# Optimization experiments

Measured on AMD Instinct MI355X. Metric: run time of the kernel, lower is better.

The kernel has to match this reference:

```python
import jax, jax.numpy as jnp
import numpy as np

N, E, D, H = 50000, 800000, 128, 64


def _norm_adj(edge_index, num_nodes):
    # add self loops, then w_ij = d_i^{-1/2} d_j^{-1/2} with deg = in-degree of col
    loops = jnp.arange(num_nodes)
    row = jnp.concatenate([edge_index[0], loops])
    col = jnp.concatenate([edge_index[1], loops])
    deg = jax.ops.segment_sum(jnp.ones_like(col, dtype=jnp.float32), col, num_segments=num_nodes)
    dinv = jnp.where(deg > 0, jax.lax.rsqrt(deg), 0.0)
    w = dinv[row] * dinv[col]
    return row, col, w


def _spmm(row, col, w, x, num_nodes):
    # y[row] += w * x[col]  (torch.sparse.mm(adj, x))
    return jax.ops.segment_sum(w[:, None] * x[col], row, num_segments=num_nodes)


def setup_inputs() -> dict:
    key = jax.random.key(0)
    ks = jax.random.split(key, 8)
    inp = {
        "x": jax.random.normal(ks[0], (N, D), dtype=jnp.float32),
        "edge_index": jax.random.randint(ks[1], (2, E), 0, N),
        "num_nodes": N,
    }
    # per-branch, per-layer Linear weights stored as [in, hid] (x @ W)
    wk = jax.random.split(ks[2], 6)
    s = 0.05
    inp["homo_W0"] = jax.random.normal(wk[0], (D, H), dtype=jnp.float32) * s
    inp["homo_W1"] = jax.random.normal(wk[1], (H, H), dtype=jnp.float32) * s
    inp["full_W0"] = jax.random.normal(wk[2], (D, H), dtype=jnp.float32) * s
    inp["full_W1"] = jax.random.normal(wk[3], (H, H), dtype=jnp.float32) * s
    inp["het_W0"] = jax.random.normal(wk[4], (D, H), dtype=jnp.float32) * s
    inp["het_W1"] = jax.random.normal(wk[5], (H, H), dtype=jnp.float32) * s
    for name in ("homo_a0", "homo_a1", "full_a0", "full_a1", "het_a0", "het_a1",
                 "w_homo", "w_full", "w_hetero"):
        inp[name] = jnp.float32(1.0)
    return inp


def reference(x, edge_index, num_nodes,
              homo_W0, homo_W1, full_W0, full_W1, het_W0, het_W1,
              homo_a0, homo_a1, full_a0, full_a1, het_a0, het_a1,
              w_homo, w_full, w_hetero):
    row, col, w = _norm_adj(edge_index, num_nodes)

    def homo_layer(h, W, a):
        return jax.nn.relu(a * (_spmm(row, col, w, h, num_nodes) @ W))

    def full_layer(h, W, a):
        return jax.nn.relu(a * (h @ W))

    def het_layer(h, W, a):
        # L = I - A  =>  L @ h = h - A @ h
        return jax.nn.relu(a * ((h - _spmm(row, col, w, h, num_nodes)) @ W))

    h_homo = homo_layer(homo_layer(x, homo_W0, homo_a0), homo_W1, homo_a1)
    h_full = full_layer(full_layer(x, full_W0, full_a0), full_W1, full_a1)
    h_het = het_layer(het_layer(x, het_W0, het_a0), het_W1, het_a1)
    combined = w_homo * h_homo + w_full * h_full + w_hetero * h_het
    return (combined, h_homo, h_full, h_het)
```

## Files before the change

kernel.cpp:

```cpp
#include <hip/hip_runtime.h>


typedef __attribute__((ext_vector_type(8))) short short8;
typedef __attribute__((ext_vector_type(4))) float f32x4;

static __device__ __forceinline__ unsigned short f2bf(float f) {
    unsigned int u = __float_as_uint(f);
    u += 0x7FFFu + ((u >> 16) & 1u);
    return (unsigned short)(u >> 16);
}
static __device__ __forceinline__ float bflo(unsigned int pv) {
    return __uint_as_float(pv << 16);
}
static __device__ __forceinline__ float bfhi(unsigned int pv) {
    return __uint_as_float(pv & 0xFFFF0000u);
}

#define PSHIFT 7
#define PSIZE  128
#define NPART_MAX 400
#define PCAP   3072
#define ACHUNK 6272

__global__ __launch_bounds__(256) void wpackT_kernel(
    const float* __restrict__ w0, const float* __restrict__ w1,
    const float* __restrict__ w2, unsigned short* __restrict__ out)
{
    const int i = blockIdx.x * 256 + threadIdx.x;
    if (i >= 3 * 64 * 128) return;
    const int b   = i >> 13;
    const int col = (i >> 7) & 63;
    const int k   = i & 127;
    const float* __restrict__ w = (b == 0) ? w0 : ((b == 1) ? w1 : w2);
    out[i] = f2bf(w[k * 64 + col]);
}

__global__ __launch_bounds__(256) void radix_kernel(
    const int* __restrict__ ei, int E, int npart,
    int* __restrict__ gcnt_r, int* __restrict__ gcnt_c,
    unsigned int* __restrict__ rbuf, unsigned short* __restrict__ cbuf)
{
    __shared__ int hist_r[NPART_MAX], lofs_r[NPART_MAX], resv_r[NPART_MAX];
    __shared__ int hist_c[NPART_MAX], lofs_c[NPART_MAX], resv_c[NPART_MAX];
    __shared__ int seg_r[16], seg_c[16];
    __shared__ unsigned int   sr[ACHUNK];
    __shared__ unsigned short sc[ACHUNK];
    const int tid = threadIdx.x;
    const int e0 = blockIdx.x * ACHUNK;
    const int e1 = (e0 + ACHUNK < E) ? e0 + ACHUNK : E;
    const int cnt = e1 - e0;
    if (cnt <= 0) return;

    for (int i = tid; i < npart; i += 256) { hist_r[i] = 0; hist_c[i] = 0; }
    __syncthreads();

    for (int e = e0 + tid; e < e1; e += 256) {
        const int r = ei[e], c = ei[E + e];
        atomicAdd(&hist_r[r >> PSHIFT], 1);
        atomicAdd(&hist_c[c >> PSHIFT], 1);
    }
    __syncthreads();

    const int SEG = (npart + 7) / 8;
    if (tid < 8) {
        int s = 0;
        const int a = tid * SEG, b = (a + SEG < npart) ? a + SEG : npart;
        for (int i = a; i < b; ++i) { lofs_r[i] = s; s += hist_r[i]; }
        seg_r[tid] = s;
    } else if (tid >= 64 && tid < 72) {
        const int t = tid - 64;
        int s = 0;
        const int a = t * SEG, b = (a + SEG < npart) ? a + SEG : npart;
        for (int i = a; i < b; ++i) { lofs_c[i] = s; s += hist_c[i]; }
        seg_c[t] = s;
    }
    __syncthreads();
    if (tid == 0) {
        int s = 0;
        for (int k = 0; k < 8; ++k) { const int t = seg_r[k]; seg_r[k] = s; s += t; }
    } else if (tid == 64) {
        int s = 0;
        for (int k = 0; k < 8; ++k) { const int t = seg_c[k]; seg_c[k] = s; s += t; }
    }
    __syncthreads();
    for (int i = tid; i < npart; i += 256) {
        lofs_r[i] += seg_r[i / SEG];
        lofs_c[i] += seg_c[i / SEG];
    }
    __syncthreads();

    for (int i = tid; i < npart; i += 256) {
        resv_r[i] = atomicAdd(&gcnt_r[i], hist_r[i]);
        resv_c[i] = atomicAdd(&gcnt_c[i], hist_c[i]);
        hist_r[i] = 0; hist_c[i] = 0;
    }
    __syncthreads();

    for (int e = e0 + tid; e < e1; e += 256) {
        const int r = ei[e], c = ei[E + e];
        const int pr = r >> PSHIFT, pc = c >> PSHIFT;
        const int jr = lofs_r[pr] + atomicAdd(&hist_r[pr], 1);
        const int jc = lofs_c[pc] + atomicAdd(&hist_c[pc], 1);
        sr[jr] = ((unsigned int)r << 16) | (unsigned int)c;
        sc[jc] = (unsigned short)c;
    }
    __syncthreads();

    for (int j = tid; j < cnt; j += 256) {
        const unsigned int rc = sr[j];
        const int p = (int)(rc >> 16) >> PSHIFT;
        const int idx = resv_r[p] + (j - lofs_r[p]);
        if (idx < PCAP) rbuf[(size_t)p * PCAP + idx] = rc;
    }
    for (int j = tid; j < cnt; j += 256) {
        const unsigned short cv = sc[j];
        const int p = (int)cv >> PSHIFT;
        const int idx = resv_c[p] + (j - lofs_c[p]);
        if (idx < PCAP) cbuf[(size_t)p * PCAP + idx] = cv;
    }
}

__global__ __launch_bounds__(256) void bucket_kernel(
    const unsigned int* __restrict__ rbuf, const unsigned short* __restrict__ cbuf,
    const int* __restrict__ gcnt_r, const int* __restrict__ gcnt_c, int N,
    unsigned short* __restrict__ bucket, int* __restrict__ cur,
    float* __restrict__ dinv)
{
    __shared__ unsigned short sbucket[PSIZE * 64];
    __shared__ int scur[PSIZE], sdeg[PSIZE];
    const int tid = threadIdx.x;
    const int p = blockIdx.x;
    const int lo = p << PSHIFT;
    const int sl = (lo + PSIZE < N) ? PSIZE : N - lo;
    if (sl <= 0) return;

    for (int i = tid; i < sl; i += 256) { scur[i] = 0; sdeg[i] = 0; }
    __syncthreads();

    int cnt_r = gcnt_r[p]; if (cnt_r > PCAP) cnt_r = PCAP;
    int cnt_c = gcnt_c[p]; if (cnt_c > PCAP) cnt_c = PCAP;

    for (int e = tid; e < cnt_r; e += 256) {
        const unsigned int rc = rbuf[(size_t)p * PCAP + e];
        const int local = (int)(rc >> 16) - lo;
        const int pos = atomicAdd(&scur[local], 1);
        if (pos < 64) sbucket[local * 64 + pos] = (unsigned short)(rc & 0xFFFFu);
    }
    for (int e = tid; e < cnt_c; e += 256) {
        atomicAdd(&sdeg[(int)cbuf[(size_t)p * PCAP + e] - lo], 1);
    }
    __syncthreads();

    for (int i = tid; i < sl; i += 256) {
        cur[lo + i]  = scur[i];
        dinv[lo + i] = 1.0f / sqrtf((float)sdeg[i] + 1.0f);
    }
    unsigned int* gb = (unsigned int*)(bucket + (size_t)lo * 64);
    const unsigned int* sb = (const unsigned int*)sbucket;
    for (int i = tid; i < sl * 32; i += 256) gb[i] = sb[i];
}

__global__ __launch_bounds__(256) void gemm_l1_kernel(
    const float* __restrict__ x, const unsigned short* __restrict__ Wt,
    unsigned short* __restrict__ Pb, float* __restrict__ full1,
    const float* __restrict__ alphaF, int N)
{
    __shared__ __align__(16) unsigned short sx[64 * 136];
    const int tid = threadIdx.x;
    const int row0 = blockIdx.x * 64;

    #pragma unroll
    for (int j = 0; j < 8; ++j) {
        const int idx = j * 256 + tid;
        const int row = idx >> 5;
        const int c4  = idx & 31;
        float4 v = make_float4(0.f, 0.f, 0.f, 0.f);
        if (row0 + row < N) v = ((const float4*)x)[(size_t)(row0 + row) * 32 + c4];
        const unsigned int lo = (unsigned int)f2bf(v.x) | ((unsigned int)f2bf(v.y) << 16);
        const unsigned int hi = (unsigned int)f2bf(v.z) | ((unsigned int)f2bf(v.w) << 16);
        *(uint2*)&sx[row * 136 + c4 * 4] = make_uint2(lo, hi);
    }
    __syncthreads();

    const int lane = tid & 63;
    const int w = tid >> 6;
    const int g = lane >> 4;
    const int m = lane & 15;
    const float alpha = alphaF[0];

    short8 afr[4];
    #pragma unroll
    for (int kk = 0; kk < 4; ++kk)
        afr[kk] = *(const short8*)&sx[(16 * w + m) * 136 + kk * 32 + g * 8];

    const int rbase = row0 + 16 * w + g * 4;

    #pragma unroll 1
    for (int b = 0; b < 3; ++b) {
        const unsigned short* __restrict__ Wb = Wt + b * 8192;
        f32x4 acc0 = {0.f, 0.f, 0.f, 0.f};
        f32x4 acc1 = {0.f, 0.f, 0.f, 0.f};
        f32x4 acc2 = {0.f, 0.f, 0.f, 0.f};
        f32x4 acc3 = {0.f, 0.f, 0.f, 0.f};
        #pragma unroll
        for (int kk = 0; kk < 4; ++kk) {
            const unsigned short* wk = Wb + m * 128 + kk * 32 + g * 8;
            const short8 b0 = *(const short8*)(wk);
            const short8 b1 = *(const short8*)(wk + 16 * 128);
            const short8 b2 = *(const short8*)(wk + 32 * 128);
            const short8 b3 = *(const short8*)(wk + 48 * 128);
            acc0 = __builtin_amdgcn_mfma_f32_16x16x32_bf16(afr[kk], b0, acc0, 0, 0, 0);
            acc1 = __builtin_amdgcn_mfma_f32_16x16x32_bf16(afr[kk], b1, acc1, 0, 0, 0);
            acc2 = __builtin_amdgcn_mfma_f32_16x16x32_bf16(afr[kk], b2, acc2, 0, 0, 0);
            acc3 = __builtin_amdgcn_mfma_f32_16x16x32_bf16(afr[kk], b3, acc3, 0, 0, 0);
        }
        #pragma unroll
        for (int j = 0; j < 4; ++j) {
            const int row = rbase + j;
            if (row < N) {
                if (b < 2) {
                    unsigned short* p = Pb + (size_t)row * 128 + b * 64 + m;
                    p[0]  = f2bf(acc0[j]);
                    p[16] = f2bf(acc1[j]);
                    p[32] = f2bf(acc2[j]);
                    p[48] = f2bf(acc3[j]);
                } else {
                    float* p = full1 + (size_t)row * 64 + m;
                    p[0]  = fmaxf(alpha * acc0[j], 0.f);
                    p[16] = fmaxf(alpha * acc1[j], 0.f);
                    p[32] = fmaxf(alpha * acc2[j], 0.f);
                    p[48] = fmaxf(alpha * acc3[j], 0.f);
                }
            }
        }
    }
}

__global__ __launch_bounds__(256) void gemm_l2_kernel(
    const float* __restrict__ in0, const float* __restrict__ in1,
    const float* __restrict__ in2,
    const float* __restrict__ w0, const float* __restrict__ w1,
    const float* __restrict__ w2,
    unsigned short* __restrict__ Qb, float* __restrict__ outF,
    const float* __restrict__ alphaF, int N)
{
    __shared__ float sxT[64][129];
    __shared__ float sW[64 * 64];
    const int b = blockIdx.y;
    const float* __restrict__ in = (b == 0) ? in0 : ((b == 1) ? in1 : in2);
    const float* __restrict__ W  = (b == 0) ? w0  : ((b == 1) ? w1  : w2);
    const int tid = threadIdx.x;
    const int row0 = blockIdx.x * 128;

    {
        const float4* __restrict__ w4 = (const float4*)W;
        float4* sw4 = (float4*)sW;
        #pragma unroll
        for (int j = 0; j < 4; ++j) sw4[j * 256 + tid] = w4[j * 256 + tid];
    }
    if (row0 + 128 <= N) {
        const float4* __restrict__ in4 = (const float4*)(in + (size_t)row0 * 64);
        #pragma unroll
        for (int j = 0; j < 8; ++j) {
            const int idx = j * 256 + tid;
            const int row = idx >> 4;
            const int kc4 = idx & 15;
            const float4 v = in4[idx];
            sxT[4 * kc4 + 0][row] = v.x;
            sxT[4 * kc4 + 1][row] = v.y;
            sxT[4 * kc4 + 2][row] = v.z;
            sxT[4 * kc4 + 3][row] = v.w;
        }
    } else {
        for (int j = 0; j < 8; ++j) {
            const int idx = j * 256 + tid;
            const int row = idx >> 4;
            const int kc4 = idx & 15;
            float4 v = make_float4(0.f, 0.f, 0.f, 0.f);
            if (row0 + row < N) v = ((const float4*)in)[(size_t)(row0 + row) * 16 + kc4];
            sxT[4 * kc4 + 0][row] = v.x;
            sxT[4 * kc4 + 1][row] = v.y;
            sxT[4 * kc4 + 2][row] = v.z;
            sxT[4 * kc4 + 3][row] = v.w;
        }
    }
    __syncthreads();

    const int tx = tid & 15;
    const int ty = tid >> 4;
    float acc[8][4];
    #pragma unroll
    for (int r = 0; r < 8; ++r)
        #pragma unroll
        for (int c = 0; c < 4; ++c) acc[r][c] = 0.f;

    #pragma unroll 2
    for (int k = 0; k < 64; ++k) {
        const float4 wv = *(const float4*)&sW[k * 64 + 4 * tx];
        const float4 xa = *(const float4*)&sxT[k][8 * ty];
        const float4 xb = *(const float4*)&sxT[k][8 * ty + 4];
        const float xr[8] = { xa.x, xa.y, xa.z, xa.w, xb.x, xb.y, xb.z, xb.w };
        #pragma unroll
        for (int r = 0; r < 8; ++r) {
            acc[r][0] = fmaf(xr[r], wv.x, acc[r][0]);
            acc[r][1] = fmaf(xr[r], wv.y, acc[r][1]);
            acc[r][2] = fmaf(xr[r], wv.z, acc[r][2]);
            acc[r][3] = fmaf(xr[r], wv.w, acc[r][3]);
        }
    }

    const float alpha = alphaF[0];
    #pragma unroll
    for (int r = 0; r < 8; ++r) {
        const int row = row0 + 8 * ty + r;
        if (row < N) {
            if (b < 2) {
                uint2 o;
                o.x = (unsigned int)f2bf(acc[r][0]) | ((unsigned int)f2bf(acc[r][1]) << 16);
                o.y = (unsigned int)f2bf(acc[r][2]) | ((unsigned int)f2bf(acc[r][3]) << 16);
                ((uint2*)Qb)[(size_t)row * 32 + b * 16 + tx] = o;
            } else {
                float4 o = make_float4(fmaxf(alpha * acc[r][0], 0.f),
                                       fmaxf(alpha * acc[r][1], 0.f),
                                       fmaxf(alpha * acc[r][2], 0.f),
                                       fmaxf(alpha * acc[r][3], 0.f));
                ((float4*)outF)[(size_t)row * 16 + tx] = o;
            }
        }
    }
}

__global__ __launch_bounds__(256) void spmm1_kernel(
    const unsigned short* __restrict__ Pb, const unsigned short* __restrict__ bucket,
    const int* __restrict__ cnt, const float* __restrict__ dinv,
    float* __restrict__ homo1, float* __restrict__ het1,
    const float* __restrict__ aH, const float* __restrict__ aT, int N)
{
    const int i = blockIdx.x * 4 + (threadIdx.x >> 6);
    if (i >= N) return;
    const int lane = threadIdx.x & 63;
    const int g  = lane >> 4;
    const int fl = lane & 15;
    const uint4* __restrict__ P16 = (const uint4*)Pb;
    const float di = dinv[i];
    const uint4 us = P16[(size_t)i * 16 + fl];
    float ps[8];
    ps[0] = bflo(us.x); ps[1] = bfhi(us.x); ps[2] = bflo(us.y); ps[3] = bfhi(us.y);
    ps[4] = bflo(us.z); ps[5] = bfhi(us.z); ps[6] = bflo(us.w); ps[7] = bfhi(us.w);
    int n = cnt[i]; if (n > 64) n = 64;
    const unsigned int* __restrict__ bp = (const unsigned int*)(bucket + (size_t)i * 64);
    float acc[8];
    #pragma unroll
    for (int j = 0; j < 8; ++j) acc[j] = 0.f;
    for (int k0 = 0; k0 < n; k0 += 4) {
        const int k = k0 + g;
        const unsigned int pw = bp[(k0 >> 1) + (g >> 1)];
        const bool act = (k < n);
        const int craw = (int)((g & 1) ? (pw >> 16) : (pw & 0xFFFFu));
        const int c = act ? craw : i;
        const float dc = act ? dinv[c] : 0.f;
        const uint4 u = P16[(size_t)c * 16 + fl];
        acc[0] = fmaf(dc, bflo(u.x), acc[0]); acc[1] = fmaf(dc, bfhi(u.x), acc[1]);
        acc[2] = fmaf(dc, bflo(u.y), acc[2]); acc[3] = fmaf(dc, bfhi(u.y), acc[3]);
        acc[4] = fmaf(dc, bflo(u.z), acc[4]); acc[5] = fmaf(dc, bfhi(u.z), acc[5]);
        acc[6] = fmaf(dc, bflo(u.w), acc[6]); acc[7] = fmaf(dc, bfhi(u.w), acc[7]);
    }
    float y[8];
    #pragma unroll
    for (int j = 0; j < 8; ++j) {
        acc[j] += __shfl_xor(acc[j], 16);
        acc[j] += __shfl_xor(acc[j], 32);
        y[j] = di * (acc[j] + di * ps[j]);
    }
    if (lane < 8) {
        const float a = aH[0];
        float4* dst = (float4*)(homo1 + (size_t)i * 64 + 8 * lane);
        dst[0] = make_float4(fmaxf(a * y[0], 0.f), fmaxf(a * y[1], 0.f),
                             fmaxf(a * y[2], 0.f), fmaxf(a * y[3], 0.f));
        dst[1] = make_float4(fmaxf(a * y[4], 0.f), fmaxf(a * y[5], 0.f),
                             fmaxf(a * y[6], 0.f), fmaxf(a * y[7], 0.f));
    } else if (lane < 16) {
        const float a = aT[0];
        float4* dst = (float4*)(het1 + (size_t)i * 64 + 8 * (lane - 8));
        dst[0] = make_float4(fmaxf(a * (ps[0] - y[0]), 0.f), fmaxf(a * (ps[1] - y[1]), 0.f),
                             fmaxf(a * (ps[2] - y[2]), 0.f), fmaxf(a * (ps[3] - y[3]), 0.f));
        dst[1] = make_float4(fmaxf(a * (ps[4] - y[4]), 0.f), fmaxf(a * (ps[5] - y[5]), 0.f),
                             fmaxf(a * (ps[6] - y[6]), 0.f), fmaxf(a * (ps[7] - y[7]), 0.f));
    }
}

__global__ __launch_bounds__(256) void spmm2_kernel(
    const unsigned short* __restrict__ Qb, const unsigned short* __restrict__ bucket,
    const int* __restrict__ cnt, const float* __restrict__ dinv,
    const float* __restrict__ full2,
    float* __restrict__ outComb, float* __restrict__ outHomo, float* __restrict__ outHet,
    const float* __restrict__ aH, const float* __restrict__ aT,
    const float* __restrict__ wH, const float* __restrict__ wF, const float* __restrict__ wT,
    int N)
{
    const int i = blockIdx.x * 4 + (threadIdx.x >> 6);
    if (i >= N) return;
    const int lane = threadIdx.x & 63;
    const int g  = lane >> 4;
    const int fl = lane & 15;
    const uint4* __restrict__ Q16 = (const uint4*)Qb;
    const float di = dinv[i];
    const uint4 us = Q16[(size_t)i * 16 + fl];
    float ps[8];
    ps[0] = bflo(us.x); ps[1] = bfhi(us.x); ps[2] = bflo(us.y); ps[3] = bfhi(us.y);
    ps[4] = bflo(us.z); ps[5] = bfhi(us.z); ps[6] = bflo(us.w); ps[7] = bfhi(us.w);
    int n = cnt[i]; if (n > 64) n = 64;
    const unsigned int* __restrict__ bp = (const unsigned int*)(bucket + (size_t)i * 64);
    float acc[8];
    #pragma unroll
    for (int j = 0; j < 8; ++j) acc[j] = 0.f;
    for (int k0 = 0; k0 < n; k0 += 4) {
        const int k = k0 + g;
        const unsigned int pw = bp[(k0 >> 1) + (g >> 1)];
        const bool act = (k < n);
        const int craw = (int)((g & 1) ? (pw >> 16) : (pw & 0xFFFFu));
        const int c = act ? craw : i;
        const float dc = act ? dinv[c] : 0.f;
        const uint4 u = Q16[(size_t)c * 16 + fl];
        acc[0] = fmaf(dc, bflo(u.x), acc[0]); acc[1] = fmaf(dc, bfhi(u.x), acc[1]);
        acc[2] = fmaf(dc, bflo(u.y), acc[2]); acc[3] = fmaf(dc, bfhi(u.y), acc[3]);
        acc[4] = fmaf(dc, bflo(u.z), acc[4]); acc[5] = fmaf(dc, bfhi(u.z), acc[5]);
        acc[6] = fmaf(dc, bflo(u.w), acc[6]); acc[7] = fmaf(dc, bfhi(u.w), acc[7]);
    }
    float y[8];
    #pragma unroll
    for (int j = 0; j < 8; ++j) {
        acc[j] += __shfl_xor(acc[j], 16);
        acc[j] += __shfl_xor(acc[j], 32);
        y[j] = di * (acc[j] + di * ps[j]);
    }
    float v[8];
    if (fl < 8) {
        const float a = aH[0];
        #pragma unroll
        for (int j = 0; j < 8; ++j) v[j] = fmaxf(a * y[j], 0.f);
    } else {
        const float a = aT[0];
        #pragma unroll
        for (int j = 0; j < 8; ++j) v[j] = fmaxf(a * (ps[j] - y[j]), 0.f);
    }
    if (lane < 8) {
        float4* dst = (float4*)(outHomo + (size_t)i * 64 + 8 * lane);
        dst[0] = make_float4(v[0], v[1], v[2], v[3]);
        dst[1] = make_float4(v[4], v[5], v[6], v[7]);
    } else if (lane < 16) {
        float4* dst = (float4*)(outHet + (size_t)i * 64 + 8 * (lane - 8));
        dst[0] = make_float4(v[0], v[1], v[2], v[3]);
        dst[1] = make_float4(v[4], v[5], v[6], v[7]);
    }
    float t[8];
    #pragma unroll
    for (int j = 0; j < 8; ++j) t[j] = __shfl_xor(v[j], 8);
    if (lane < 8) {
        const float4* f4 = (const float4*)(full2 + (size_t)i * 64 + 8 * lane);
        const float4 fa = f4[0], fb = f4[1];
        const float cwh = wH[0], cwf = wF[0], cwt = wT[0];
        float4* dst = (float4*)(outComb + (size_t)i * 64 + 8 * lane);
        dst[0] = make_float4(cwh * v[0] + cwf * fa.x + cwt * t[0],
                             cwh * v[1] + cwf * fa.y + cwt * t[1],
                             cwh * v[2] + cwf * fa.z + cwt * t[2],
                             cwh * v[3] + cwf * fa.w + cwt * t[3]);
        dst[1] = make_float4(cwh * v[4] + cwf * fb.x + cwt * t[4],
                             cwh * v[5] + cwf * fb.y + cwt * t[5],
                             cwh * v[6] + cwf * fb.z + cwt * t[6],
                             cwh * v[7] + cwf * fb.w + cwt * t[7]);
    }
}

extern "C" void kernel_launch(void* const* d_in, const int* in_sizes, int n_in,
                              void* d_out, int out_size, void* d_ws, size_t ws_size,
                              hipStream_t stream)
{
    const float* x  = (const float*)d_in[0];
    const int*   ei = (const int*)d_in[1];
    const int N = in_sizes[0] / 128;
    const int E = in_sizes[1] / 2;
    const float* homo_W0 = (const float*)d_in[3];
    const float* homo_W1 = (const float*)d_in[4];
    const float* full_W0 = (const float*)d_in[5];
    const float* full_W1 = (const float*)d_in[6];
    const float* het_W0  = (const float*)d_in[7];
    const float* het_W1  = (const float*)d_in[8];
    const float* homo_a0 = (const float*)d_in[9];
    const float* homo_a1 = (const float*)d_in[10];
    const float* full_a0 = (const float*)d_in[11];
    const float* full_a1 = (const float*)d_in[12];
    const float* het_a0  = (const float*)d_in[13];
    const float* het_a1  = (const float*)d_in[14];
    const float* w_homo  = (const float*)d_in[15];
    const float* w_full  = (const float*)d_in[16];
    const float* w_het   = (const float*)d_in[17];

    char* ws = (char*)d_ws;
    size_t off = 0;
    auto alloc = [&](size_t bytes) -> char* {
        char* p = ws + off;
        off = (off + bytes + 511) & ~(size_t)511;
        return p;
    };
    int*            cur    = (int*)alloc((size_t)N * 4);
    float*          dinv   = (float*)alloc((size_t)N * 4);
    unsigned short* bucket = (unsigned short*)alloc((size_t)N * 64 * 2);
    int*            gcnt   = (int*)alloc((size_t)2 * NPART_MAX * 4);
    unsigned short* Wt     = (unsigned short*)alloc((size_t)3 * 64 * 128 * 2);
    const size_t rbuf_sz = (size_t)NPART_MAX * PCAP * 4;
    const size_t cbuf_sz = (size_t)NPART_MAX * PCAP * 2;
    size_t unionA_sz = (size_t)N * 128 * 2;
    if (rbuf_sz + cbuf_sz > unionA_sz) unionA_sz = rbuf_sz + cbuf_sz;
    char*           unionA = alloc(unionA_sz);
    unsigned int*   rbuf   = (unsigned int*)unionA;
    unsigned short* cbuf   = (unsigned short*)(unionA + rbuf_sz);
    unsigned short* Pb     = (unsigned short*)unionA;
    float*          full1  = (float*)alloc((size_t)N * 64 * 4);
    float*          homo1  = (float*)alloc((size_t)N * 64 * 4);
    float*          het1   = (float*)alloc((size_t)N * 64 * 4);
    unsigned short* Qb     = Pb;

    float* out      = (float*)d_out;
    float* outComb  = out;
    float* outHomo  = out + (size_t)N * 64;
    float* outFull  = out + (size_t)2 * N * 64;
    float* outHet   = out + (size_t)3 * N * 64;

    const int npart = (N + PSIZE - 1) >> PSHIFT;

    hipMemsetAsync(gcnt, 0, (size_t)2 * NPART_MAX * 4, stream);

    wpackT_kernel<<<(3 * 64 * 128 + 255) / 256, 256, 0, stream>>>(
        homo_W0, het_W0, full_W0, Wt);

    const int ablocks = (E + ACHUNK - 1) / ACHUNK;
    radix_kernel<<<ablocks, 256, 0, stream>>>(
        ei, E, npart, gcnt, gcnt + NPART_MAX, rbuf, cbuf);
    bucket_kernel<<<npart, 256, 0, stream>>>(
        rbuf, cbuf, gcnt, gcnt + NPART_MAX, N, bucket, cur, dinv);

    gemm_l1_kernel<<<(N + 63) / 64, 256, 0, stream>>>(
        x, Wt, Pb, full1, full_a0, N);
    spmm1_kernel<<<(N + 3) / 4, 256, 0, stream>>>(
        Pb, bucket, cur, dinv, homo1, het1, homo_a0, het_a0, N);

    gemm_l2_kernel<<<dim3((N + 127) / 128, 3), 256, 0, stream>>>(
        homo1, het1, full1, homo_W1, het_W1, full_W1, Qb, outFull, full_a1, N);
    spmm2_kernel<<<(N + 3) / 4, 256, 0, stream>>>(
        Qb, bucket, cur, dinv, outFull, outComb, outHomo, outHet,
        homo_a1, het_a1, w_homo, w_full, w_het, N);
}
```

Measured before the change: 180.2 us.

## Prescale by dinv in GEMM epilogues, bf16 intermediates, MFMA layer-2 GEMM

The GEMM epilogues now multiply source rows by dinv, so the SpMM gather no longer loads dinv per neighbour. The heterophilic branch recovers the unscaled value by dividing by di. Layer-1 intermediates (homo1, het1, full1) are stored as bf16 rather than fp32, which halves their memory traffic. The scalar FP32 layer-2 GEMM is replaced by one bf16 MFMA kernel that handles all three branches per block, using weights pre-packed in the wpack kernel. This adds more bf16 rounding error to the intermediates.

```diff
diff --git a/kernel.cpp b/kernel.cpp
--- a/kernel.cpp
+++ b/kernel.cpp
@@ -23,16 +23,23 @@
 #define ACHUNK 6272
 
 __global__ __launch_bounds__(256) void wpackT_kernel(
-    const float* __restrict__ w0, const float* __restrict__ w1,
-    const float* __restrict__ w2, unsigned short* __restrict__ out)
+    const float* __restrict__ w10, const float* __restrict__ w11,
+    const float* __restrict__ w12, const float* __restrict__ w20,
+    const float* __restrict__ w21, const float* __restrict__ w22,
+    unsigned short* __restrict__ out)
 {
     const int i = blockIdx.x * 256 + threadIdx.x;
-    if (i >= 3 * 64 * 128) return;
-    const int b   = i >> 13;
-    const int col = (i >> 7) & 63;
-    const int k   = i & 127;
-    const float* __restrict__ w = (b == 0) ? w0 : ((b == 1) ? w1 : w2);
-    out[i] = f2bf(w[k * 64 + col]);
+    const int L1 = 3 * 64 * 128;
+    if (i < L1) {
+        const int b = i >> 13, col = (i >> 7) & 63, k = i & 127;
+        const float* __restrict__ w = (b == 0) ? w10 : ((b == 1) ? w11 : w12);
+        out[i] = f2bf(w[k * 64 + col]);
+    } else if (i < L1 + 3 * 64 * 64) {
+        const int j = i - L1;
+        const int b = j >> 12, col = (j >> 6) & 63, k = j & 63;
+        const float* __restrict__ w = (b == 0) ? w20 : ((b == 1) ? w21 : w22);
+        out[i] = f2bf(w[k * 64 + col]);
+    }
 }
 
 __global__ __launch_bounds__(256) void radix_kernel(
@@ -162,7 +169,8 @@
 
 __global__ __launch_bounds__(256) void gemm_l1_kernel(
     const float* __restrict__ x, const unsigned short* __restrict__ Wt,
-    unsigned short* __restrict__ Pb, float* __restrict__ full1,
+    const float* __restrict__ dinv,
+    unsigned short* __restrict__ Pb, unsigned short* __restrict__ full1b,
     const float* __restrict__ alphaF, int N)
 {
     __shared__ __align__(16) unsigned short sx[64 * 136];
@@ -194,6 +202,10 @@
         afr[kk] = *(const short8*)&sx[(16 * w + m) * 136 + kk * 32 + g * 8];
 
     const int rbase = row0 + 16 * w + g * 4;
+    float dv[4];
+    #pragma unroll
+    for (int j = 0; j < 4; ++j)
+        dv[j] = (rbase + j < N) ? dinv[rbase + j] : 0.f;
 
     #pragma unroll 1
     for (int b = 0; b < 3; ++b) {
@@ -220,12 +232,92 @@
             if (row < N) {
                 if (b < 2) {
                     unsigned short* p = Pb + (size_t)row * 128 + b * 64 + m;
-                    p[0]  = f2bf(acc0[j]);
-                    p[16] = f2bf(acc1[j]);
-                    p[32] = f2bf(acc2[j]);
-                    p[48] = f2bf(acc3[j]);
+                    p[0]  = f2bf(dv[j] * acc0[j]);
+                    p[16] = f2bf(dv[j] * acc1[j]);
+                    p[32] = f2bf(dv[j] * acc2[j]);
+                    p[48] = f2bf(dv[j] * acc3[j]);
                 } else {
-                    float* p = full1 + (size_t)row * 64 + m;
+                    unsigned short* p = full1b + (size_t)row * 64 + m;
+                    p[0]  = f2bf(fmaxf(alpha * acc0[j], 0.f));
+                    p[16] = f2bf(fmaxf(alpha * acc1[j], 0.f));
+                    p[32] = f2bf(fmaxf(alpha * acc2[j], 0.f));
+                    p[48] = f2bf(fmaxf(alpha * acc3[j], 0.f));
+                }
+            }
+        }
+    }
+}
+
+__global__ __launch_bounds__(256) void gemm_l2_kernel(
+    const unsigned short* __restrict__ h1b, const unsigned short* __restrict__ t1b,
+    const unsigned short* __restrict__ f1b, const unsigned short* __restrict__ Wt2,
+    const float* __restrict__ dinv,
+    unsigned short* __restrict__ Qb, float* __restrict__ outF,
+    const float* __restrict__ alphaF, int N)
+{
+    __shared__ __align__(16) unsigned short sx[3][64 * 72];
+    const int tid = threadIdx.x;
+    const int row0 = blockIdx.x * 64;
+
+    #pragma unroll
+    for (int b = 0; b < 3; ++b) {
+        const unsigned short* __restrict__ in = (b == 0) ? h1b : ((b == 1) ? t1b : f1b);
+        #pragma unroll
+        for (int j = 0; j < 2; ++j) {
+            const int idx = j * 256 + tid;
+            const int row = idx >> 3, seg = idx & 7;
+            uint4 v = make_uint4(0, 0, 0, 0);
+            if (row0 + row < N) v = ((const uint4*)in)[(size_t)(row0 + row) * 8 + seg];
+            *(uint4*)&sx[b][row * 72 + seg * 8] = v;
+        }
+    }
+    __syncthreads();
+
+    const int lane = tid & 63;
+    const int w = tid >> 6;
+    const int g = lane >> 4, m = lane & 15;
+    const float alpha = alphaF[0];
+    const int rbase = row0 + 16 * w + g * 4;
+
+    float dv[4];
+    #pragma unroll
+    for (int j = 0; j < 4; ++j)
+        dv[j] = (rbase + j < N) ? dinv[rbase + j] : 0.f;
+
+    #pragma unroll 1
+    for (int b = 0; b < 3; ++b) {
+        const short8 afr0 = *(const short8*)&sx[b][(16 * w + m) * 72 + g * 8];
+        const short8 afr1 = *(const short8*)&sx[b][(16 * w + m) * 72 + 32 + g * 8];
+        const unsigned short* __restrict__ Wb = Wt2 + b * 4096;
+        f32x4 acc0 = {0.f, 0.f, 0.f, 0.f};
+        f32x4 acc1 = {0.f, 0.f, 0.f, 0.f};
+        f32x4 acc2 = {0.f, 0.f, 0.f, 0.f};
+        f32x4 acc3 = {0.f, 0.f, 0.f, 0.f};
+        #pragma unroll
+        for (int kk = 0; kk < 2; ++kk) {
+            const short8 af = kk ? afr1 : afr0;
+            const unsigned short* wk = Wb + m * 64 + kk * 32 + g * 8;
+            const short8 b0 = *(const short8*)(wk);
+            const short8 b1 = *(const short8*)(wk + 16 * 64);
+            const short8 b2 = *(const short8*)(wk + 32 * 64);
+            const short8 b3 = *(const short8*)(wk + 48 * 64);
+            acc0 = __builtin_amdgcn_mfma_f32_16x16x32_bf16(af, b0, acc0, 0, 0, 0);
+            acc1 = __builtin_amdgcn_mfma_f32_16x16x32_bf16(af, b1, acc1, 0, 0, 0);
+            acc2 = __builtin_amdgcn_mfma_f32_16x16x32_bf16(af, b2, acc2, 0, 0, 0);
+            acc3 = __builtin_amdgcn_mfma_f32_16x16x32_bf16(af, b3, acc3, 0, 0, 0);
+        }
+        #pragma unroll
+        for (int j = 0; j < 4; ++j) {
+            const int row = rbase + j;
+            if (row < N) {
+                if (b < 2) {
+                    unsigned short* p = Qb + (size_t)row * 128 + b * 64 + m;
+                    p[0]  = f2bf(dv[j] * acc0[j]);
+                    p[16] = f2bf(dv[j] * acc1[j]);
+                    p[32] = f2bf(dv[j] * acc2[j]);
+                    p[48] = f2bf(dv[j] * acc3[j]);
+                } else {
+                    float* p = outF + (size_t)row * 64 + m;
                     p[0]  = fmaxf(alpha * acc0[j], 0.f);
                     p[16] = fmaxf(alpha * acc1[j], 0.f);
                     p[32] = fmaxf(alpha * acc2[j], 0.f);
@@ -236,104 +328,10 @@
     }
 }
 
-__global__ __launch_bounds__(256) void gemm_l2_kernel(
-    const float* __restrict__ in0, const float* __restrict__ in1,
-    const float* __restrict__ in2,
-    const float* __restrict__ w0, const float* __restrict__ w1,
-    const float* __restrict__ w2,
-    unsigned short* __restrict__ Qb, float* __restrict__ outF,
-    const float* __restrict__ alphaF, int N)
-{
-    __shared__ float sxT[64][129];
-    __shared__ float sW[64 * 64];
-    const int b = blockIdx.y;
-    const float* __restrict__ in = (b == 0) ? in0 : ((b == 1) ? in1 : in2);
-    const float* __restrict__ W  = (b == 0) ? w0  : ((b == 1) ? w1  : w2);
-    const int tid = threadIdx.x;
-    const int row0 = blockIdx.x * 128;
-
-    {
-        const float4* __restrict__ w4 = (const float4*)W;
-        float4* sw4 = (float4*)sW;
-        #pragma unroll
-        for (int j = 0; j < 4; ++j) sw4[j * 256 + tid] = w4[j * 256 + tid];
-    }
-    if (row0 + 128 <= N) {
-        const float4* __restrict__ in4 = (const float4*)(in + (size_t)row0 * 64);
-        #pragma unroll
-        for (int j = 0; j < 8; ++j) {
-            const int idx = j * 256 + tid;
-            const int row = idx >> 4;
-            const int kc4 = idx & 15;
-            const float4 v = in4[idx];
-            sxT[4 * kc4 + 0][row] = v.x;
-            sxT[4 * kc4 + 1][row] = v.y;
-            sxT[4 * kc4 + 2][row] = v.z;
-            sxT[4 * kc4 + 3][row] = v.w;
-        }
-    } else {
-        for (int j = 0; j < 8; ++j) {
-            const int idx = j * 256 + tid;
-            const int row = idx >> 4;
-            const int kc4 = idx & 15;
-            float4 v = make_float4(0.f, 0.f, 0.f, 0.f);
-            if (row0 + row < N) v = ((const float4*)in)[(size_t)(row0 + row) * 16 + kc4];
-            sxT[4 * kc4 + 0][row] = v.x;
-            sxT[4 * kc4 + 1][row] = v.y;
-            sxT[4 * kc4 + 2][row] = v.z;
-            sxT[4 * kc4 + 3][row] = v.w;
-        }
-    }
-    __syncthreads();
-
-    const int tx = tid & 15;
-    const int ty = tid >> 4;
-    float acc[8][4];
-    #pragma unroll
-    for (int r = 0; r < 8; ++r)
-        #pragma unroll
-        for (int c = 0; c < 4; ++c) acc[r][c] = 0.f;
-
-    #pragma unroll 2
-    for (int k = 0; k < 64; ++k) {
-        const float4 wv = *(const float4*)&sW[k * 64 + 4 * tx];
-        const float4 xa = *(const float4*)&sxT[k][8 * ty];
-        const float4 xb = *(const float4*)&sxT[k][8 * ty + 4];
-        const float xr[8] = { xa.x, xa.y, xa.z, xa.w, xb.x, xb.y, xb.z, xb.w };
-        #pragma unroll
-        for (int r = 0; r < 8; ++r) {
-            acc[r][0] = fmaf(xr[r], wv.x, acc[r][0]);
-            acc[r][1] = fmaf(xr[r], wv.y, acc[r][1]);
-            acc[r][2] = fmaf(xr[r], wv.z, acc[r][2]);
-            acc[r][3] = fmaf(xr[r], wv.w, acc[r][3]);
-        }
-    }
-
-    const float alpha = alphaF[0];
-    #pragma unroll
-    for (int r = 0; r < 8; ++r) {
-        const int row = row0 + 8 * ty + r;
-        if (row < N) {
-            if (b < 2) {
-                uint2 o;
-                o.x = (unsigned int)f2bf(acc[r][0]) | ((unsigned int)f2bf(acc[r][1]) << 16);
-                o.y = (unsigned int)f2bf(acc[r][2]) | ((unsigned int)f2bf(acc[r][3]) << 16);
-                ((uint2*)Qb)[(size_t)row * 32 + b * 16 + tx] = o;
-            } else {
-                float4 o = make_float4(fmaxf(alpha * acc[r][0], 0.f),
-                                       fmaxf(alpha * acc[r][1], 0.f),
-                                       fmaxf(alpha * acc[r][2], 0.f),
-                                       fmaxf(alpha * acc[r][3], 0.f));
-                ((float4*)outF)[(size_t)row * 16 + tx] = o;
-            }
-        }
-    }
-}
-
 __global__ __launch_bounds__(256) void spmm1_kernel(
     const unsigned short* __restrict__ Pb, const unsigned short* __restrict__ bucket,
     const int* __restrict__ cnt, const float* __restrict__ dinv,
-    float* __restrict__ homo1, float* __restrict__ het1,
+    unsigned short* __restrict__ homo1b, unsigned short* __restrict__ het1b,
     const float* __restrict__ aH, const float* __restrict__ aT, int N)
 {
     const int i = blockIdx.x * 4 + (threadIdx.x >> 6);
@@ -355,37 +353,46 @@
     for (int k0 = 0; k0 < n; k0 += 4) {
         const int k = k0 + g;
         const unsigned int pw = bp[(k0 >> 1) + (g >> 1)];
-        const bool act = (k < n);
+        const float s = (k < n) ? 1.0f : 0.0f;
         const int craw = (int)((g & 1) ? (pw >> 16) : (pw & 0xFFFFu));
-        const int c = act ? craw : i;
-        const float dc = act ? dinv[c] : 0.f;
+        const int c = (k < n) ? craw : i;
         const uint4 u = P16[(size_t)c * 16 + fl];
-        acc[0] = fmaf(dc, bflo(u.x), acc[0]); acc[1] = fmaf(dc, bfhi(u.x), acc[1]);
-        acc[2] = fmaf(dc, bflo(u.y), acc[2]); acc[3] = fmaf(dc, bfhi(u.y), acc[3]);
-        acc[4] = fmaf(dc, bflo(u.z), acc[4]); acc[5] = fmaf(dc, bfhi(u.z), acc[5]);
-        acc[6] = fmaf(dc, bflo(u.w), acc[6]); acc[7] = fmaf(dc, bfhi(u.w), acc[7]);
+        acc[0] = fmaf(s, bflo(u.x), acc[0]); acc[1] = fmaf(s, bfhi(u.x), acc[1]);
+        acc[2] = fmaf(s, bflo(u.y), acc[2]); acc[3] = fmaf(s, bfhi(u.y), acc[3]);
+        acc[4] = fmaf(s, bflo(u.z), acc[4]); acc[5] = fmaf(s, bfhi(u.z), acc[5]);
+        acc[6] = fmaf(s, bflo(u.w), acc[6]); acc[7] = fmaf(s, bfhi(u.w), acc[7]);
     }
     float y[8];
     #pragma unroll
     for (int j = 0; j < 8; ++j) {
         acc[j] += __shfl_xor(acc[j], 16);
         acc[j] += __shfl_xor(acc[j], 32);
-        y[j] = di * (acc[j] + di * ps[j]);
+        y[j] = di * (acc[j] + ps[j]);
     }
     if (lane < 8) {
         const float a = aH[0];
-        float4* dst = (float4*)(homo1 + (size_t)i * 64 + 8 * lane);
-        dst[0] = make_float4(fmaxf(a * y[0], 0.f), fmaxf(a * y[1], 0.f),
-                             fmaxf(a * y[2], 0.f), fmaxf(a * y[3], 0.f));
-        dst[1] = make_float4(fmaxf(a * y[4], 0.f), fmaxf(a * y[5], 0.f),
-                             fmaxf(a * y[6], 0.f), fmaxf(a * y[7], 0.f));
+        uint4 o;
+        o.x = (unsigned int)f2bf(fmaxf(a * y[0], 0.f)) |
+              ((unsigned int)f2bf(fmaxf(a * y[1], 0.f)) << 16);
+        o.y = (unsigned int)f2bf(fmaxf(a * y[2], 0.f)) |
+              ((unsigned int)f2bf(fmaxf(a * y[3], 0.f)) << 16);
+        o.z = (unsigned int)f2bf(fmaxf(a * y[4], 0.f)) |
+              ((unsigned int)f2bf(fmaxf(a * y[5], 0.f)) << 16);
+        o.w = (unsigned int)f2bf(fmaxf(a * y[6], 0.f)) |
+              ((unsigned int)f2bf(fmaxf(a * y[7], 0.f)) << 16);
+        ((uint4*)homo1b)[(size_t)i * 8 + lane] = o;
     } else if (lane < 16) {
         const float a = aT[0];
-        float4* dst = (float4*)(het1 + (size_t)i * 64 + 8 * (lane - 8));
-        dst[0] = make_float4(fmaxf(a * (ps[0] - y[0]), 0.f), fmaxf(a * (ps[1] - y[1]), 0.f),
-                             fmaxf(a * (ps[2] - y[2]), 0.f), fmaxf(a * (ps[3] - y[3]), 0.f));
-        dst[1] = make_float4(fmaxf(a * (ps[4] - y[4]), 0.f), fmaxf(a * (ps[5] - y[5]), 0.f),
-                             fmaxf(a * (ps[6] - y[6]), 0.f), fmaxf(a * (ps[7] - y[7]), 0.f));
+        const float rdi = 1.0f / di;
+        float v[8];
+        #pragma unroll
+        for (int j = 0; j < 8; ++j) v[j] = fmaxf(a * (ps[j] * rdi - y[j]), 0.f);
+        uint4 o;
+        o.x = (unsigned int)f2bf(v[0]) | ((unsigned int)f2bf(v[1]) << 16);
+        o.y = (unsigned int)f2bf(v[2]) | ((unsigned int)f2bf(v[3]) << 16);
+        o.z = (unsigned int)f2bf(v[4]) | ((unsigned int)f2bf(v[5]) << 16);
+        o.w = (unsigned int)f2bf(v[6]) | ((unsigned int)f2bf(v[7]) << 16);
+        ((uint4*)het1b)[(size_t)i * 8 + (lane - 8)] = o;
     }
 }
 
@@ -417,22 +424,21 @@
     for (int k0 = 0; k0 < n; k0 += 4) {
         const int k = k0 + g;
         const unsigned int pw = bp[(k0 >> 1) + (g >> 1)];
-        const bool act = (k < n);
+        const float s = (k < n) ? 1.0f : 0.0f;
         const int craw = (int)((g & 1) ? (pw >> 16) : (pw & 0xFFFFu));
-        const int c = act ? craw : i;
-        const float dc = act ? dinv[c] : 0.f;
+        const int c = (k < n) ? craw : i;
         const uint4 u = Q16[(size_t)c * 16 + fl];
-        acc[0] = fmaf(dc, bflo(u.x), acc[0]); acc[1] = fmaf(dc, bfhi(u.x), acc[1]);
-        acc[2] = fmaf(dc, bflo(u.y), acc[2]); acc[3] = fmaf(dc, bfhi(u.y), acc[3]);
-        acc[4] = fmaf(dc, bflo(u.z), acc[4]); acc[5] = fmaf(dc, bfhi(u.z), acc[5]);
-        acc[6] = fmaf(dc, bflo(u.w), acc[6]); acc[7] = fmaf(dc, bfhi(u.w), acc[7]);
+        acc[0] = fmaf(s, bflo(u.x), acc[0]); acc[1] = fmaf(s, bfhi(u.x), acc[1]);
+        acc[2] = fmaf(s, bflo(u.y), acc[2]); acc[3] = fmaf(s, bfhi(u.y), acc[3]);
+        acc[4] = fmaf(s, bflo(u.z), acc[4]); acc[5] = fmaf(s, bfhi(u.z), acc[5]);
+        acc[6] = fmaf(s, bflo(u.w), acc[6]); acc[7] = fmaf(s, bfhi(u.w), acc[7]);
     }
     float y[8];
     #pragma unroll
     for (int j = 0; j < 8; ++j) {
         acc[j] += __shfl_xor(acc[j], 16);
         acc[j] += __shfl_xor(acc[j], 32);
-        y[j] = di * (acc[j] + di * ps[j]);
+        y[j] = di * (acc[j] + ps[j]);
     }
     float v[8];
     if (fl < 8) {
@@ -441,8 +447,9 @@
         for (int j = 0; j < 8; ++j) v[j] = fmaxf(a * y[j], 0.f);
     } else {
         const float a = aT[0];
-        #pragma unroll
-        for (int j = 0; j < 8; ++j) v[j] = fmaxf(a * (ps[j] - y[j]), 0.f);
+        const float rdi = 1.0f / di;
+        #pragma unroll
+        for (int j = 0; j < 8; ++j) v[j] = fmaxf(a * (ps[j] * rdi - y[j]), 0.f);
     }
     if (lane < 8) {
         float4* dst = (float4*)(outHomo + (size_t)i * 64 + 8 * lane);
@@ -507,7 +514,7 @@
     float*          dinv   = (float*)alloc((size_t)N * 4);
     unsigned short* bucket = (unsigned short*)alloc((size_t)N * 64 * 2);
     int*            gcnt   = (int*)alloc((size_t)2 * NPART_MAX * 4);
-    unsigned short* Wt     = (unsigned short*)alloc((size_t)3 * 64 * 128 * 2);
+    unsigned short* Wt     = (unsigned short*)alloc((size_t)(3 * 64 * 128 + 3 * 64 * 64) * 2);
     const size_t rbuf_sz = (size_t)NPART_MAX * PCAP * 4;
     const size_t cbuf_sz = (size_t)NPART_MAX * PCAP * 2;
     size_t unionA_sz = (size_t)N * 128 * 2;
@@ -516,9 +523,9 @@
     unsigned int*   rbuf   = (unsigned int*)unionA;
     unsigned short* cbuf   = (unsigned short*)(unionA + rbuf_sz);
     unsigned short* Pb     = (unsigned short*)unionA;
-    float*          full1  = (float*)alloc((size_t)N * 64 * 4);
-    float*          homo1  = (float*)alloc((size_t)N * 64 * 4);
-    float*          het1   = (float*)alloc((size_t)N * 64 * 4);
+    unsigned short* full1b = (unsigned short*)alloc((size_t)N * 64 * 2);
+    unsigned short* homo1b = (unsigned short*)alloc((size_t)N * 64 * 2);
+    unsigned short* het1b  = (unsigned short*)alloc((size_t)N * 64 * 2);
     unsigned short* Qb     = Pb;
 
     float* out      = (float*)d_out;
@@ -531,8 +538,8 @@
 
     hipMemsetAsync(gcnt, 0, (size_t)2 * NPART_MAX * 4, stream);
 
-    wpackT_kernel<<<(3 * 64 * 128 + 255) / 256, 256, 0, stream>>>(
-        homo_W0, het_W0, full_W0, Wt);
+    wpackT_kernel<<<(3 * 64 * 128 + 3 * 64 * 64 + 255) / 256, 256, 0, stream>>>(
+        homo_W0, het_W0, full_W0, homo_W1, het_W1, full_W1, Wt);
 
     const int ablocks = (E + ACHUNK - 1) / ACHUNK;
     radix_kernel<<<ablocks, 256, 0, stream>>>(
@@ -541,12 +548,12 @@
         rbuf, cbuf, gcnt, gcnt + NPART_MAX, N, bucket, cur, dinv);
 
     gemm_l1_kernel<<<(N + 63) / 64, 256, 0, stream>>>(
-        x, Wt, Pb, full1, full_a0, N);
+        x, Wt, dinv, Pb, full1b, full_a0, N);
     spmm1_kernel<<<(N + 3) / 4, 256, 0, stream>>>(
-        Pb, bucket, cur, dinv, homo1, het1, homo_a0, het_a0, N);
-
-    gemm_l2_kernel<<<dim3((N + 127) / 128, 3), 256, 0, stream>>>(
-        homo1, het1, full1, homo_W1, het_W1, full_W1, Qb, outFull, full_a1, N);
+        Pb, bucket, cur, dinv, homo1b, het1b, homo_a0, het_a0, N);
+
+    gemm_l2_kernel<<<(N + 63) / 64, 256, 0, stream>>>(
+        homo1b, het1b, full1b, Wt + 3 * 64 * 128, dinv, Qb, outFull, full_a1, N);
     spmm2_kernel<<<(N + 3) / 4, 256, 0, stream>>>(
         Qb, bucket, cur, dinv, outFull, outComb, outHomo, outHet,
         homo_a1, het_a1, w_homo, w_full, w_het, N);
```

After: 174.6 us. 1.03x faster.
